# Kernel tuning notes

Measured on AMD Instinct MI355X. Metric: run time of the kernel, lower is better.

Reference implementation:

```python
import jax, jax.numpy as jnp
import numpy as np

B, V, H, W, CIN, COUT = 2, 4, 256, 256, 64, 64
WINDOW = 1
GAMMA = 0.1


def setup_inputs() -> dict:
    key = jax.random.key(0)
    ks = jax.random.split(key, 6)
    # gaussian positions: x,y in [-1,1], z in [0.5,2.5] so projection masks are nontrivial
    means = jax.random.uniform(ks[0], (B, V, H, W, 3), dtype=jnp.float32)
    means = means * jnp.array([2.0, 2.0, 2.0], jnp.float32) + jnp.array([-1.0, -1.0, 0.5], jnp.float32)
    depths = jax.random.uniform(ks[1], (B, V, H, W, 1, 1), dtype=jnp.float32)
    gs_feats = jax.random.normal(ks[2], (B, V, H, W, CIN), dtype=jnp.float32)
    # normalized intrinsics (ndc in [0,1))
    intr = jnp.array([[0.8, 0.0, 0.5], [0.0, 0.8, 0.5], [0.0, 0.0, 1.0]], jnp.float32)
    intrinsics = jnp.broadcast_to(intr, (B, V, 3, 3))
    # camera-to-world extrinsics: identity rotation, small per-view translations
    t = jax.random.uniform(ks[3], (B, V, 3), minval=-0.2, maxval=0.2, dtype=jnp.float32)
    extrinsics = jnp.broadcast_to(jnp.eye(4, dtype=jnp.float32), (B, V, 4, 4)).at[..., :3, 3].set(t)
    w1 = jax.random.normal(ks[4], (COUT, CIN, 3, 3), dtype=jnp.float32) * 0.05
    b1 = jnp.zeros((COUT,), jnp.float32)
    w2 = jax.random.normal(ks[5], (COUT, COUT, 3, 3), dtype=jnp.float32) * 0.05
    b2 = jnp.zeros((COUT,), jnp.float32)
    return {"means": means, "depths": depths, "gs_feats": gs_feats,
            "intrinsics": intrinsics, "extrinsics": extrinsics,
            "w1": w1, "b1": b1, "w2": w2, "b2": b2}


def _project(points, intr, extr, eps=1e-8):
    # points (b, n, 3) world; extr (b,4,4) cam-to-world; intr (b,3,3) normalized
    w2c = jnp.linalg.inv(extr)
    ph = jnp.concatenate([points, jnp.ones_like(points[..., :1])], axis=-1)  # (b,n,4)
    cam = jnp.einsum('bij,bnj->bni', w2c, ph)[..., :3]
    z = cam[..., 2:3]
    ndc = jnp.einsum('bij,bnj->bni', intr, cam / (z + eps))
    return ndc[..., :2], cam[..., 2] > eps


def _conv3x3(x, w, b):
    y = jax.lax.conv_general_dilated(x, w, (1, 1), 'SAME',
                                     dimension_numbers=('NCHW', 'OIHW', 'NCHW'))
    return y + b[None, :, None, None]


def reference(means, depths, gs_feats, intrinsics, extrinsics, w1, b1, w2, b2):
    b, v, h, w_, c = gs_feats.shape
    hw = h * w_
    feats_flat = gs_feats.reshape(b, v, hw, c)
    pts = means.reshape(b, v, hw, 3)
    outs = []
    for j in range(v):
        acc = feats_flat[:, j]                      # (b, hw, c)
        norm = jnp.ones((b,), gs_feats.dtype)
        for k in range(v):
            if j != k and (k - WINDOW) <= j <= (k + WINDOW):
                ndc, valid_z = _project(pts[:, j], intrinsics[:, k], extrinsics[:, k])
                px = jnp.floor(ndc[..., 0] * w_).astype(jnp.int32)
                py = jnp.floor(ndc[..., 1] * h).astype(jnp.int32)
                mask = ((ndc[..., 0] >= 0) & (ndc[..., 0] < 1) &
                        (ndc[..., 1] >= 0) & (ndc[..., 1] < 1) & valid_z)  # (b,hw)
                idx = jnp.clip(py, 0, h - 1) * w_ + jnp.clip(px, 0, w_ - 1)
                gathered = jnp.take_along_axis(feats_flat[:, k], idx[..., None], axis=1)
                upd = jnp.where(mask[..., None], gathered, jnp.zeros((), gs_feats.dtype))
                scale = GAMMA * mask.sum(-1).astype(gs_feats.dtype) / (h * w_)  # (b,)
                acc = acc + upd * scale[:, None, None]
                norm = norm + scale
        outs.append(acc / norm[:, None, None])
    fused = jnp.stack(outs, axis=1).reshape(b * v, h, w_, c).transpose(0, 3, 1, 2)  # (bv,c,h,w)
    x = _conv3x3(fused, w1, b1)
    x = jax.nn.gelu(x, approximate=False)
    x = _conv3x3(x, w2, b2)
    return x.transpose(0, 2, 3, 1).reshape(b, v, h, w_, -1)
```

## Files before the change

kernel.cpp:

```cpp
#include <hip/hip_runtime.h>
#include <math.h>

#define HW 65536
#define NPAD 258

typedef short bf16x8 __attribute__((ext_vector_type(8)));
typedef float f32x4  __attribute__((ext_vector_type(4)));

#define O_COUNTS 0
#define O_W2C    2048
#define O_WT     4096
#define O_META   151552
#define O_FUSED  3297280
#define O_X1     71458816

#define ROWPX 66
#define ROWB  (ROWPX * 128)
#define ROWSTR (ROWB + 16)
#define ROWSTRS (ROWSTR / 2)

__device__ __forceinline__ unsigned short f2bf(float f) {
    unsigned int u = __float_as_uint(f);
    u += 0x7FFFu + ((u >> 16) & 1u);
    return (unsigned short)(u >> 16);
}

__global__ __launch_bounds__(256) void prep_kernel(
    const float* __restrict__ extr, const float* __restrict__ w1,
    const float* __restrict__ w2, float* __restrict__ w2c,
    unsigned short* __restrict__ wT, unsigned short* __restrict__ fusedP,
    unsigned short* __restrict__ x1P, int* __restrict__ counts)
{
    int tid = blockIdx.x * blockDim.x + threadIdx.x;
    int nth = gridDim.x * blockDim.x;

    if (blockIdx.x == 0) {
        if (threadIdx.x < 8) {
            float a[4][8];
            const float* E = extr + threadIdx.x * 16;
            for (int r = 0; r < 4; r++)
                for (int c = 0; c < 4; c++) {
                    a[r][c] = E[r*4 + c];
                    a[r][4+c] = (r == c) ? 1.0f : 0.0f;
                }
            for (int col = 0; col < 4; col++) {
                int piv = col; float bm = fabsf(a[col][col]);
                for (int r = col+1; r < 4; r++) {
                    float v = fabsf(a[r][col]);
                    if (v > bm) { bm = v; piv = r; }
                }
                if (piv != col)
                    for (int c = 0; c < 8; c++) { float t = a[col][c]; a[col][c] = a[piv][c]; a[piv][c] = t; }
                float f = 1.0f / a[col][col];
                for (int c = 0; c < 8; c++) a[col][c] *= f;
                for (int r = 0; r < 4; r++) if (r != col) {
                    float f2 = a[r][col];
                    for (int c = 0; c < 8; c++) a[r][c] -= f2 * a[col][c];
                }
            }
            float* O = w2c + threadIdx.x * 16;
            for (int r = 0; r < 4; r++)
                for (int c = 0; c < 4; c++) O[r*4+c] = a[r][4+c];
        }
    }

    for (int i = tid; i < 384; i += nth) counts[i] = 0;

    for (int e = tid; e < 73728; e += nth) {
        int t = e;
        int j  = t & 7;  t >>= 3;
        int co = t & 63; t >>= 6;
        int q  = t & 3;  t >>= 2;
        int tap = t % 9; t /= 9;
        int h  = t & 1;  int cv = t >> 1;
        int ci = h*32 + q*8 + j;
        int ky = tap / 3, kx = tap % 3;
        const float* wsrc = cv ? w2 : w1;
        float v = wsrc[((co*64 + ci)*3 + ky)*3 + kx];
        wT[cv*36864 + ((((h*9 + tap)*4 + q)*64 + co)*8 + j)] = f2bf(v);
    }

    for (int u = tid; u < 2*8*1028*8; u += nth) {
        int t = u;
        int ch   = t & 7;    t >>= 3;
        int cell = t % 1028; t /= 1028;
        int n    = t & 7;    int buf = t >> 3;
        int y, x;
        if      (cell < 258) { y = 0;   x = cell; }
        else if (cell < 516) { y = 257; x = cell - 258; }
        else if (cell < 772) { y = cell - 516 + 1; x = 0; }
        else                 { y = cell - 772 + 1; x = 257; }
        unsigned short* p = (buf ? x1P : fusedP) +
            (((size_t)(n*NPAD + y)*NPAD + x)*64 + ch*8);
        *reinterpret_cast<uint4*>(p) = make_uint4(0u, 0u, 0u, 0u);
    }
}

__global__ __launch_bounds__(256) void proj_kernel(
    const float* __restrict__ means, const float* __restrict__ intr,
    const float* __restrict__ w2c, int* __restrict__ meta,
    int* __restrict__ counts)
{
    const int jt[6] = {0,1,1,2,2,3};
    const int kt[6] = {1,0,2,1,3,2};
    int s = blockIdx.y;
    int b = s / 6, p = s % 6;
    int j = jt[p], k = kt[p];
    int i = blockIdx.x * 256 + threadIdx.x;

    __shared__ int bcnt;
    if (threadIdx.x == 0) bcnt = 0;
    __syncthreads();

    const float* mp = means + ((size_t)(b*4 + j)*HW + i)*3;
    float x = mp[0], y = mp[1], z = mp[2];
    const float* M = w2c + (b*4 + k)*16;
    const float* I = intr + (b*4 + k)*9;

    float cx = fmaf(M[2],  z, fmaf(M[1], y, M[0]*x)) + M[3];
    float cy = fmaf(M[6],  z, fmaf(M[5], y, M[4]*x)) + M[7];
    float cz = fmaf(M[10], z, fmaf(M[9], y, M[8]*x)) + M[11];

    bool vz = cz > 1e-8f;
    float zi = cz + 1e-8f;
    float sx = cx / zi, sy = cy / zi, sz = cz / zi;
    float nx = fmaf(I[2], sz, fmaf(I[1], sy, I[0]*sx));
    float ny = fmaf(I[5], sz, fmaf(I[4], sy, I[3]*sx));

    int px = (int)floorf(nx * 256.0f);
    int py = (int)floorf(ny * 256.0f);
    bool mask = (nx >= 0.0f) && (nx < 1.0f) && (ny >= 0.0f) && (ny < 1.0f) && vz;
    int pxc = min(max(px, 0), 255);
    int pyc = min(max(py, 0), 255);
    int idx = pyc*256 + pxc;
    meta[(size_t)s*HW + i] = idx | (mask ? (int)0x80000000 : 0);

    unsigned long long bal = __ballot(mask ? 1 : 0);
    if ((threadIdx.x & 63) == 0)
        atomicAdd(&bcnt, (int)__popcll(bal));
    __syncthreads();
    if (threadIdx.x == 0)
        atomicAdd(counts + s*32, bcnt);
}

__global__ __launch_bounds__(256) void fuse_kernel(
    const float* __restrict__ feats, const int* __restrict__ meta,
    const int* __restrict__ counts, unsigned short* __restrict__ fusedP)
{
    const int nsl[4]    = {1, 2, 2, 1};
    const int slt[4][2] = {{0,0},{1,2},{3,4},{5,5}};
    const int kvw[4][2] = {{1,1},{0,2},{1,3},{2,2}};

    int bj = blockIdx.y;
    int b = bj >> 2, j = bj & 3;
    int pt = blockIdx.x * 16 + (threadIdx.x >> 4);
    int cg = threadIdx.x & 15;

    const float4* fj = reinterpret_cast<const float4*>(
        feats + ((size_t)bj*HW + pt)*64) + cg;
    float4 acc = *fj;
    float norm = 1.0f;
    int ns = nsl[j];
    for (int e = 0; e < 2; e++) {
        if (e < ns) {
            int p = slt[j][e], k = kvw[j][e];
            int s = b*6 + p;
            float scale = 0.1f * (float)counts[s*32] / 65536.0f;
            int mt = meta[(size_t)s*HW + pt];
            if (mt < 0) {
                int idx = mt & 0xFFFF;
                const float4* g = reinterpret_cast<const float4*>(
                    feats + ((size_t)(b*4 + k)*HW + idx)*64) + cg;
                float4 gv = *g;
                acc.x += scale * gv.x; acc.y += scale * gv.y;
                acc.z += scale * gv.z; acc.w += scale * gv.w;
            }
            norm += scale;
        }
    }
    float ox = acc.x / norm, oy = acc.y / norm;
    float oz = acc.z / norm, ow = acc.w / norm;

    int yy = pt >> 8, xx = pt & 255;
    unsigned short* op = fusedP +
        (((size_t)bj*NPAD + (yy+1))*NPAD + (xx+1))*64 + cg*4;
    ushort4 o = make_ushort4(f2bf(ox), f2bf(oy), f2bf(oz), f2bf(ow));
    *reinterpret_cast<ushort4*>(op) = o;
}

template<int MODE>
__global__ __launch_bounds__(256) void conv_kernel(
    const unsigned short* __restrict__ in, const unsigned short* __restrict__ wT,
    const float* __restrict__ bias, void* __restrict__ outp)
{
    __shared__ unsigned short smem[6 * ROWSTRS];

    int n = blockIdx.z;
    int y0 = blockIdx.y * 4;
    int X0 = blockIdx.x * 64;
    int w  = threadIdx.x >> 6;
    int lane = threadIdx.x & 63;
    int m = lane & 15, q = lane >> 4;

    int sub = lane >> 3;
    int ch8 = lane & 7;
    int srcoff = sub*128 + (((ch8 ^ sub) & 7) << 4);
    int tpx = lane >> 5;
    int tch = (lane >> 2) & 7;
    int tsrc = 8192 + tpx*128 + ((((tch ^ tpx) & 7)) << 4) + (lane & 3)*4;

    for (int ri = w; ri < 6; ri += 4) {
        const char* g = (const char*)(in + ((size_t)(n*NPAD + y0 + ri)*NPAD + X0)*64);
        char* l = (char*)smem + ri*ROWSTR;
#pragma unroll
        for (int i = 0; i < 8; i++)
            __builtin_amdgcn_global_load_lds(
                (const __attribute__((address_space(1))) unsigned int*)(g + i*1024 + srcoff),
                (__attribute__((address_space(3))) unsigned int*)(l + i*1024 + (size_t)lane*16),
                16, 0, 0);
        __builtin_amdgcn_global_load_lds(
            (const __attribute__((address_space(1))) unsigned int*)(g + tsrc),
            (__attribute__((address_space(3))) unsigned int*)(l + 8192 + (size_t)lane*4),
            4, 0, 0);
    }
    __syncthreads();

    int rowb = w * ROWSTR;
    int vb[2][3];
#pragma unroll
    for (int h = 0; h < 2; h++)
#pragma unroll
        for (int dx = 0; dx < 3; dx++)
            vb[h][dx] = rowb + m*128 + ((((h*4 + q) ^ ((m + dx) & 7)) & 7) << 4);

    f32x4 acc[4][4];
#pragma unroll
    for (int a = 0; a < 4; a++)
#pragma unroll
        for (int bq = 0; bq < 4; bq++)
            acc[a][bq] = (f32x4){0.f, 0.f, 0.f, 0.f};

#pragma unroll
    for (int h = 0; h < 2; h++) {
#pragma unroll
        for (int tap = 0; tap < 9; tap++) {
            int dy = tap/3, dx = tap%3;
            bf16x8 av[4], bv[4];
#pragma unroll
            for (int Mt = 0; Mt < 4; Mt++)
                av[Mt] = *reinterpret_cast<const bf16x8*>(
                    (const char*)smem + vb[h][dx] + dy*ROWSTR + (Mt*16 + dx)*128);
            const unsigned short* wp = wT + (size_t)(((h*9 + tap)*4 + q)*64)*8;
#pragma unroll
            for (int Nt = 0; Nt < 4; Nt++)
                bv[Nt] = *reinterpret_cast<const bf16x8*>(wp + (Nt*16 + m)*8);
#pragma unroll
            for (int Mt = 0; Mt < 4; Mt++)
#pragma unroll
                for (int Nt = 0; Nt < 4; Nt++)
                    acc[Mt][Nt] = __builtin_amdgcn_mfma_f32_16x16x32_bf16(
                        bv[Nt], av[Mt], acc[Mt][Nt], 0, 0, 0);
        }
    }

    float4 bsv[4];
#pragma unroll
    for (int Nt = 0; Nt < 4; Nt++)
        bsv[Nt] = *reinterpret_cast<const float4*>(bias + Nt*16 + q*4);

#pragma unroll
    for (int Mt = 0; Mt < 4; Mt++) {
        int px = X0 + Mt*16 + m;
#pragma unroll
        for (int Nt = 0; Nt < 4; Nt++) {
            int co0 = Nt*16 + q*4;
            float v0 = acc[Mt][Nt][0] + bsv[Nt].x;
            float v1 = acc[Mt][Nt][1] + bsv[Nt].y;
            float v2 = acc[Mt][Nt][2] + bsv[Nt].z;
            float v3 = acc[Mt][Nt][3] + bsv[Nt].w;
            if (MODE == 1) {
                v0 = 0.5f * v0 * (1.0f + erff(v0 * 0.70710678118654752f));
                v1 = 0.5f * v1 * (1.0f + erff(v1 * 0.70710678118654752f));
                v2 = 0.5f * v2 * (1.0f + erff(v2 * 0.70710678118654752f));
                v3 = 0.5f * v3 * (1.0f + erff(v3 * 0.70710678118654752f));
                unsigned short* o = (unsigned short*)outp +
                    ((size_t)(n*NPAD + y0 + w + 1)*NPAD + (px + 1))*64 + co0;
                ushort4 pk = make_ushort4(f2bf(v0), f2bf(v1), f2bf(v2), f2bf(v3));
                *reinterpret_cast<ushort4*>(o) = pk;
            } else {
                float* o = (float*)outp +
                    ((size_t)(n*256 + y0 + w)*256 + px)*64 + co0;
                *reinterpret_cast<float4*>(o) = make_float4(v0, v1, v2, v3);
            }
        }
    }
}

extern "C" void kernel_launch(void* const* d_in, const int* in_sizes, int n_in,
                              void* d_out, int out_size, void* d_ws, size_t ws_size,
                              hipStream_t stream)
{
    const float* means = (const float*)d_in[0];
    const float* feats = (const float*)d_in[2];
    const float* intr  = (const float*)d_in[3];
    const float* extr  = (const float*)d_in[4];
    const float* w1    = (const float*)d_in[5];
    const float* b1    = (const float*)d_in[6];
    const float* w2    = (const float*)d_in[7];
    const float* b2    = (const float*)d_in[8];

    char* ws = (char*)d_ws;
    int*            counts = (int*)(ws + O_COUNTS);
    float*          w2c    = (float*)(ws + O_W2C);
    unsigned short* wT     = (unsigned short*)(ws + O_WT);
    int*            meta   = (int*)(ws + O_META);
    unsigned short* fusedP = (unsigned short*)(ws + O_FUSED);
    unsigned short* x1P    = (unsigned short*)(ws + O_X1);

    prep_kernel<<<dim3(96), dim3(256), 0, stream>>>(
        extr, w1, w2, w2c, wT, fusedP, x1P, counts);
    proj_kernel<<<dim3(256, 12), dim3(256), 0, stream>>>(
        means, intr, w2c, meta, counts);
    fuse_kernel<<<dim3(4096, 8), dim3(256), 0, stream>>>(
        feats, meta, counts, fusedP);
    conv_kernel<1><<<dim3(4, 64, 8), dim3(256), 0, stream>>>(
        fusedP, wT, b1, (void*)x1P);
    conv_kernel<2><<<dim3(4, 64, 8), dim3(256), 0, stream>>>(
        x1P, wT + 36864, b2, d_out);
}
```

Baseline: 397.7 us.

## Double-buffer conv input staging by channel half and process two row tiles per block

The conv kernel now stages the input in two channel halves into two LDS buffers and overlaps loading the next half or row tile with the MFMA compute on the current one. Each block covers 8 output rows in two passes, so the grid's y dimension is halved. The exact erf GELU is replaced by a polynomial approximation built on rcp and exp. This trades a small loss of GELU accuracy and extra barriers for hiding global-to-LDS latency behind compute and cheaper epilogue math.

```diff
diff --git a/kernel.cpp b/kernel.cpp
--- a/kernel.cpp
+++ b/kernel.cpp
@@ -14,15 +14,29 @@
 #define O_FUSED  3297280
 #define O_X1     71458816
 
-#define ROWPX 66
-#define ROWB  (ROWPX * 128)
-#define ROWSTR (ROWB + 16)
-#define ROWSTRS (ROWSTR / 2)
+#define HROWB   4224
+#define HROWSTR 4240
+#define HBUFB   (6 * HROWSTR)
 
 __device__ __forceinline__ unsigned short f2bf(float f) {
     unsigned int u = __float_as_uint(f);
     u += 0x7FFFu + ((u >> 16) & 1u);
     return (unsigned short)(u >> 16);
+}
+
+__device__ __forceinline__ float gelu_fast(float v) {
+    float x  = v * 0.70710678118654752f;
+    float ax = fabsf(x);
+    float t  = __builtin_amdgcn_rcpf(fmaf(0.3275911f, ax, 1.0f));
+    float p  = fmaf(t, 1.061405429f, -1.453152027f);
+    p = fmaf(t, p, 1.421413741f);
+    p = fmaf(t, p, -0.284496736f);
+    p = fmaf(t, p, 0.254829592f);
+    p = p * t;
+    float e   = __expf(-x * x);
+    float era = fmaf(-p, e, 1.0f);
+    float er  = copysignf(era, x);
+    return 0.5f * v * (1.0f + er);
 }
 
 __global__ __launch_bounds__(256) void prep_kernel(
@@ -193,55 +207,57 @@
     const unsigned short* __restrict__ in, const unsigned short* __restrict__ wT,
     const float* __restrict__ bias, void* __restrict__ outp)
 {
-    __shared__ unsigned short smem[6 * ROWSTRS];
+    __shared__ unsigned short smem[2 * HBUFB / 2];
 
     int n = blockIdx.z;
-    int y0 = blockIdx.y * 4;
+    int Y0 = blockIdx.y * 8;
     int X0 = blockIdx.x * 64;
     int w  = threadIdx.x >> 6;
     int lane = threadIdx.x & 63;
     int m = lane & 15, q = lane >> 4;
 
-    int sub = lane >> 3;
-    int ch8 = lane & 7;
-    int srcoff = sub*128 + (((ch8 ^ sub) & 7) << 4);
-    int tpx = lane >> 5;
-    int tch = (lane >> 2) & 7;
-    int tsrc = 8192 + tpx*128 + ((((tch ^ tpx) & 7)) << 4) + (lane & 3)*4;
-
-    for (int ri = w; ri < 6; ri += 4) {
-        const char* g = (const char*)(in + ((size_t)(n*NPAD + y0 + ri)*NPAD + X0)*64);
-        char* l = (char*)smem + ri*ROWSTR;
-#pragma unroll
-        for (int i = 0; i < 8; i++)
-            __builtin_amdgcn_global_load_lds(
-                (const __attribute__((address_space(1))) unsigned int*)(g + i*1024 + srcoff),
-                (__attribute__((address_space(3))) unsigned int*)(l + i*1024 + (size_t)lane*16),
-                16, 0, 0);
-        __builtin_amdgcn_global_load_lds(
-            (const __attribute__((address_space(1))) unsigned int*)(g + tsrc),
-            (__attribute__((address_space(3))) unsigned int*)(l + 8192 + (size_t)lane*4),
-            4, 0, 0);
-    }
-    __syncthreads();
-
-    int rowb = w * ROWSTR;
-    int vb[2][3];
-#pragma unroll
-    for (int h = 0; h < 2; h++)
-#pragma unroll
-        for (int dx = 0; dx < 3; dx++)
-            vb[h][dx] = rowb + m*128 + ((((h*4 + q) ^ ((m + dx) & 7)) & 7) << 4);
+    int srcl = ((lane >> 2) * 128) + ((((lane & 3) ^ ((lane >> 3) & 3)) & 3) << 4);
+    int tsrcl = 8192 + ((lane >> 2) * 128) + ((lane & 3) << 4);
+
+    int vb[3];
+#pragma unroll
+    for (int dx = 0; dx < 3; dx++)
+        vb[dx] = w*HROWSTR + m*64 + (((q ^ (((m + dx) >> 1) & 3)) & 3) << 4);
+
+    const char* gin = (const char*)in;
+
+    auto STAGE = [&](int t, int h, int buf) {
+        const char* gb = gin + (((size_t)(n*NPAD) + (size_t)(Y0 + 4*t)) * NPAD + X0) * 128 + h*64;
+        char* lb = (char*)smem + buf*HBUFB;
+        for (int ri = w; ri < 6; ri += 4) {
+            const char* g = gb + (size_t)ri * (NPAD*128);
+            char* l = lb + ri*HROWSTR;
+#pragma unroll
+            for (int i = 0; i < 4; i++)
+                __builtin_amdgcn_global_load_lds(
+                    (const __attribute__((address_space(1))) unsigned int*)(g + i*2048 + srcl),
+                    (__attribute__((address_space(3))) unsigned int*)(l + i*1024 + (size_t)lane*16),
+                    16, 0, 0);
+            if (lane < 8)
+                __builtin_amdgcn_global_load_lds(
+                    (const __attribute__((address_space(1))) unsigned int*)(g + tsrcl),
+                    (__attribute__((address_space(3))) unsigned int*)(l + 4096 + (size_t)lane*16),
+                    16, 0, 0);
+        }
+    };
 
     f32x4 acc[4][4];
-#pragma unroll
-    for (int a = 0; a < 4; a++)
-#pragma unroll
-        for (int bq = 0; bq < 4; bq++)
-            acc[a][bq] = (f32x4){0.f, 0.f, 0.f, 0.f};
-
-#pragma unroll
-    for (int h = 0; h < 2; h++) {
+    auto ACCZERO = [&]() {
+#pragma unroll
+        for (int a = 0; a < 4; a++)
+#pragma unroll
+            for (int bq = 0; bq < 4; bq++)
+                acc[a][bq] = (f32x4){0.f, 0.f, 0.f, 0.f};
+    };
+
+    auto COMPUTE = [&](int h, int buf) {
+        const char* sb = (const char*)smem + buf*HBUFB;
+        const char* wb = (const char*)wT + h*9*4096 + q*1024 + m*16;
 #pragma unroll
         for (int tap = 0; tap < 9; tap++) {
             int dy = tap/3, dx = tap%3;
@@ -249,11 +265,10 @@
 #pragma unroll
             for (int Mt = 0; Mt < 4; Mt++)
                 av[Mt] = *reinterpret_cast<const bf16x8*>(
-                    (const char*)smem + vb[h][dx] + dy*ROWSTR + (Mt*16 + dx)*128);
-            const unsigned short* wp = wT + (size_t)(((h*9 + tap)*4 + q)*64)*8;
+                    sb + vb[dx] + dy*HROWSTR + Mt*1024 + dx*64);
 #pragma unroll
             for (int Nt = 0; Nt < 4; Nt++)
-                bv[Nt] = *reinterpret_cast<const bf16x8*>(wp + (Nt*16 + m)*8);
+                bv[Nt] = *reinterpret_cast<const bf16x8*>(wb + tap*4096 + Nt*256);
 #pragma unroll
             for (int Mt = 0; Mt < 4; Mt++)
 #pragma unroll
@@ -261,39 +276,61 @@
                     acc[Mt][Nt] = __builtin_amdgcn_mfma_f32_16x16x32_bf16(
                         bv[Nt], av[Mt], acc[Mt][Nt], 0, 0, 0);
         }
-    }
+    };
 
     float4 bsv[4];
 #pragma unroll
     for (int Nt = 0; Nt < 4; Nt++)
         bsv[Nt] = *reinterpret_cast<const float4*>(bias + Nt*16 + q*4);
 
-#pragma unroll
-    for (int Mt = 0; Mt < 4; Mt++) {
-        int px = X0 + Mt*16 + m;
-#pragma unroll
-        for (int Nt = 0; Nt < 4; Nt++) {
-            int co0 = Nt*16 + q*4;
-            float v0 = acc[Mt][Nt][0] + bsv[Nt].x;
-            float v1 = acc[Mt][Nt][1] + bsv[Nt].y;
-            float v2 = acc[Mt][Nt][2] + bsv[Nt].z;
-            float v3 = acc[Mt][Nt][3] + bsv[Nt].w;
-            if (MODE == 1) {
-                v0 = 0.5f * v0 * (1.0f + erff(v0 * 0.70710678118654752f));
-                v1 = 0.5f * v1 * (1.0f + erff(v1 * 0.70710678118654752f));
-                v2 = 0.5f * v2 * (1.0f + erff(v2 * 0.70710678118654752f));
-                v3 = 0.5f * v3 * (1.0f + erff(v3 * 0.70710678118654752f));
-                unsigned short* o = (unsigned short*)outp +
-                    ((size_t)(n*NPAD + y0 + w + 1)*NPAD + (px + 1))*64 + co0;
-                ushort4 pk = make_ushort4(f2bf(v0), f2bf(v1), f2bf(v2), f2bf(v3));
-                *reinterpret_cast<ushort4*>(o) = pk;
-            } else {
-                float* o = (float*)outp +
-                    ((size_t)(n*256 + y0 + w)*256 + px)*64 + co0;
-                *reinterpret_cast<float4*>(o) = make_float4(v0, v1, v2, v3);
+    auto EPI = [&](int t) {
+        int yout = Y0 + 4*t + w;
+#pragma unroll
+        for (int Mt = 0; Mt < 4; Mt++) {
+            int px = X0 + Mt*16 + m;
+#pragma unroll
+            for (int Nt = 0; Nt < 4; Nt++) {
+                int co0 = Nt*16 + q*4;
+                float v0 = acc[Mt][Nt][0] + bsv[Nt].x;
+                float v1 = acc[Mt][Nt][1] + bsv[Nt].y;
+                float v2 = acc[Mt][Nt][2] + bsv[Nt].z;
+                float v3 = acc[Mt][Nt][3] + bsv[Nt].w;
+                if (MODE == 1) {
+                    v0 = gelu_fast(v0); v1 = gelu_fast(v1);
+                    v2 = gelu_fast(v2); v3 = gelu_fast(v3);
+                    unsigned short* o = (unsigned short*)outp +
+                        ((size_t)(n*NPAD + yout + 1)*NPAD + (px + 1))*64 + co0;
+                    ushort4 pk = make_ushort4(f2bf(v0), f2bf(v1), f2bf(v2), f2bf(v3));
+                    *reinterpret_cast<ushort4*>(o) = pk;
+                } else {
+                    float* o = (float*)outp +
+                        ((size_t)(n*256 + yout)*256 + px)*64 + co0;
+                    *reinterpret_cast<float4*>(o) = make_float4(v0, v1, v2, v3);
+                }
             }
         }
-    }
+    };
+
+    STAGE(0, 0, 0);
+    __syncthreads();
+
+    STAGE(0, 1, 1);
+    ACCZERO();
+    COMPUTE(0, 0);
+    __syncthreads();
+
+    STAGE(1, 0, 0);
+    COMPUTE(1, 1);
+    __syncthreads();
+
+    STAGE(1, 1, 1);
+    EPI(0);
+    ACCZERO();
+    COMPUTE(0, 0);
+    __syncthreads();
+
+    COMPUTE(1, 1);
+    EPI(1);
 }
 
 extern "C" void kernel_launch(void* const* d_in, const int* in_sizes, int n_in,
@@ -323,8 +360,8 @@
         means, intr, w2c, meta, counts);
     fuse_kernel<<<dim3(4096, 8), dim3(256), 0, stream>>>(
         feats, meta, counts, fusedP);
-    conv_kernel<1><<<dim3(4, 64, 8), dim3(256), 0, stream>>>(
+    conv_kernel<1><<<dim3(4, 32, 8), dim3(256), 0, stream>>>(
         fusedP, wT, b1, (void*)x1P);
-    conv_kernel<2><<<dim3(4, 64, 8), dim3(256), 0, stream>>>(
+    conv_kernel<2><<<dim3(4, 32, 8), dim3(256), 0, stream>>>(
         x1P, wT + 36864, b2, d_out);
 }
```

Result: slower. 419.2 us (+5.4%).
